# Optimization experiments

Hardware: AMD Instinct MI355X
Metric: run time of the kernel (lower is better)

## Reference

```python
import jax, jax.numpy as jnp
import numpy as np

N_NODES = 50000
HIDDEN = 256
N_EDGES = 800000


def setup_inputs() -> dict:
    key = jax.random.key(0)
    k_z, k_e, k_w1, k_b1, k_w2, k_b2 = jax.random.split(key, 6)
    z = jax.random.normal(k_z, (N_NODES, HIDDEN), dtype=jnp.float32)
    edge_index = jax.random.randint(k_e, (2, N_EDGES), 0, N_NODES, dtype=jnp.int64)
    # Linear params stored as (in, out); scaled like torch default init
    W1 = jax.random.normal(k_w1, (2 * HIDDEN, HIDDEN), dtype=jnp.float32) * (1.0 / np.sqrt(2 * HIDDEN))
    b1 = jax.random.normal(k_b1, (HIDDEN,), dtype=jnp.float32) * 0.01
    W2 = jax.random.normal(k_w2, (HIDDEN, 1), dtype=jnp.float32) * (1.0 / np.sqrt(HIDDEN))
    b2 = jax.random.normal(k_b2, (1,), dtype=jnp.float32) * 0.01
    return {"z": z, "edge_index": edge_index, "W1": W1, "b1": b1, "W2": W2, "b2": b2}


def reference(z, edge_index, W1, b1, W2, b2):
    src = edge_index[0]
    dst = edge_index[1]
    # gather endpoints and concat: [E, 2*H]
    edge_feat = jnp.concatenate([z[src], z[dst]], axis=1)
    x = jnp.dot(edge_feat, W1) + b1          # [E, H]
    x = jax.nn.relu(x)
    score = jnp.dot(x, W2) + b2              # [E, 1]
    return score
```

## Files before the change

### kernel.cpp

```cpp
#include <hip/hip_runtime.h>
#include <hip/hip_bf16.h>

#define NN 50000
#define HID 256
#define NE 800000

typedef unsigned short u16;
typedef __attribute__((ext_vector_type(8))) short short8v;
typedef __attribute__((ext_vector_type(4))) float f32x4;

__device__ __forceinline__ u16 f2bf(float v) {
    __hip_bfloat16 h = __float2bfloat16(v);
    return *reinterpret_cast<u16*>(&h);
}

__global__ __launch_bounds__(256)
void prep_w1b(const float* __restrict__ W1, u16* __restrict__ W1b) {
    const int g = blockIdx.x * 256 + threadIdx.x;
    if (g >= 2 * 32 * 256) return;
    const int h   = g >> 13;
    const int kbg = (g >> 8) & 31;
    const int jh  = g & 255;
    u16 o[8];
    #pragma unroll
    for (int kk = 0; kk < 8; ++kk)
        o[kk] = f2bf(W1[(size_t)(h * 256 + kbg * 8 + kk) * HID + jh]);
    *(uint4*)(W1b + (size_t)g * 8) = *(uint4*)o;
}

__global__ __launch_bounds__(512)
void node_gemm(const float* __restrict__ z, const u16* __restrict__ W1b,
               const float* __restrict__ b1, u16* __restrict__ P) {
    __shared__ __align__(16) u16 Blds[32 * 256 * 8];

    const int tid  = threadIdx.x;
    const int lane = tid & 63;
    const int w    = tid >> 6;
    const int l16  = lane & 15;
    const int l4   = lane >> 4;
    const int r0   = blockIdx.x * 256 + w * 32;

    short8v af[2][8];
    #pragma unroll
    for (int mi = 0; mi < 2; ++mi) {
        const int row = r0 + mi * 16 + l16;
        const bool ok = (row < NN);
        const float* zr = z + (size_t)row * HID;
        #pragma unroll
        for (int ks = 0; ks < 8; ++ks) {
            float4 v0 = make_float4(0.f, 0.f, 0.f, 0.f), v1 = v0;
            if (ok) {
                v0 = *(const float4*)(zr + ks * 32 + l4 * 8);
                v1 = *(const float4*)(zr + ks * 32 + l4 * 8 + 4);
            }
            u16 t[8] = { f2bf(v0.x), f2bf(v0.y), f2bf(v0.z), f2bf(v0.w),
                         f2bf(v1.x), f2bf(v1.y), f2bf(v1.z), f2bf(v1.w) };
            af[mi][ks] = *(short8v*)t;
        }
    }

    const uint4* Wu4 = (const uint4*)W1b;
    uint4* Lu4 = (uint4*)Blds;

    #pragma unroll
    for (int h = 0; h < 2; ++h) {
        if (h) __syncthreads();
        #pragma unroll
        for (int c = 0; c < 16; ++c)
            Lu4[c * 512 + tid] = Wu4[(size_t)h * 8192 + c * 512 + tid];
        __syncthreads();

        #pragma unroll
        for (int ni = 0; ni < 16; ++ni) {
            f32x4 acc[2] = {};
            #pragma unroll
            for (int ks = 0; ks < 8; ++ks) {
                const short8v b = *(const short8v*)
                    &Blds[((ks * 4 + l4) * 256 + ni * 16 + l16) * 8];
                #pragma unroll
                for (int mi = 0; mi < 2; ++mi)
                    acc[mi] = __builtin_amdgcn_mfma_f32_16x16x32_bf16(
                        af[mi][ks], b, acc[mi], 0, 0, 0);
            }
            const int col  = h * 256 + ni * 16 + l16;
            const float bias = (h == 0) ? b1[ni * 16 + l16] : 0.f;
            #pragma unroll
            for (int mi = 0; mi < 2; ++mi) {
                #pragma unroll
                for (int r = 0; r < 4; ++r) {
                    const int row = r0 + mi * 16 + l4 * 4 + r;
                    if (row < NN)
                        P[(size_t)row * 512 + col] = f2bf(acc[mi][r] + bias);
                }
            }
        }
    }
}

__device__ __forceinline__ void proc_pair(unsigned int ua, unsigned int ub,
                                          float w0, float w1, float& s) {
    const float a0 = __uint_as_float(ua << 16);
    const float a1 = __uint_as_float(ua & 0xffff0000u);
    const float b0 = __uint_as_float(ub << 16);
    const float b1 = __uint_as_float(ub & 0xffff0000u);
    const float x0 = fmaxf(a0 + b0, 0.f);
    const float x1 = fmaxf(a1 + b1, 0.f);
    s = fmaf(x0, w0, s);
    s = fmaf(x1, w1, s);
}

__global__ __launch_bounds__(256)
void edge_kernel(const int* __restrict__ ei, const u16* __restrict__ P,
                 const float* __restrict__ W2, const float* __restrict__ b2,
                 float* __restrict__ out) {
    const int lane = threadIdx.x & 63;
    const int sub  = lane >> 4;
    const int l16  = lane & 15;
    const int h0   = l16 * 16;

    float w[16];
    #pragma unroll
    for (int i = 0; i < 16; i += 4) {
        const float4 v = *(const float4*)(W2 + h0 + i);
        w[i] = v.x; w[i + 1] = v.y; w[i + 2] = v.z; w[i + 3] = v.w;
    }
    const float bias2 = b2[0];

    const int gwave   = (blockIdx.x * blockDim.x + threadIdx.x) >> 6;
    const int nwaves  = (gridDim.x * blockDim.x) >> 6;
    const int ngroups = NE >> 2;

    for (int g = gwave; g < ngroups; g += nwaves) {
        const int e   = g * 4 + sub;
        const int src = ei[e];
        const int dst = ei[NE + e];

        const u16* pa = P + (size_t)src * 512 + h0;
        const u16* pb = P + (size_t)dst * 512 + 256 + h0;
        const uint4 ta0 = *(const uint4*)(pa);
        const uint4 ta1 = *(const uint4*)(pa + 8);
        const uint4 tb0 = *(const uint4*)(pb);
        const uint4 tb1 = *(const uint4*)(pb + 8);

        float s = 0.f;
        proc_pair(ta0.x, tb0.x, w[0],  w[1],  s);
        proc_pair(ta0.y, tb0.y, w[2],  w[3],  s);
        proc_pair(ta0.z, tb0.z, w[4],  w[5],  s);
        proc_pair(ta0.w, tb0.w, w[6],  w[7],  s);
        proc_pair(ta1.x, tb1.x, w[8],  w[9],  s);
        proc_pair(ta1.y, tb1.y, w[10], w[11], s);
        proc_pair(ta1.z, tb1.z, w[12], w[13], s);
        proc_pair(ta1.w, tb1.w, w[14], w[15], s);

        s += __shfl_xor(s, 1);
        s += __shfl_xor(s, 2);
        s += __shfl_xor(s, 4);
        s += __shfl_xor(s, 8);
        if (l16 == 0) out[e] = s + bias2;
    }
}

extern "C" void kernel_launch(void* const* d_in, const int* in_sizes, int n_in,
                              void* d_out, int out_size, void* d_ws, size_t ws_size,
                              hipStream_t stream) {
    const float* z  = (const float*)d_in[0];
    const int*   ei = (const int*)d_in[1];
    const float* W1 = (const float*)d_in[2];
    const float* b1 = (const float*)d_in[3];
    const float* W2 = (const float*)d_in[4];
    const float* b2 = (const float*)d_in[5];
    float* out = (float*)d_out;

    u16* W1b = (u16*)d_ws;
    u16* P   = (u16*)d_ws + 131072;

    prep_w1b<<<64, 256, 0, stream>>>(W1, W1b);

    node_gemm<<<196, 512, 0, stream>>>(z, W1b, b1, P);

    edge_kernel<<<2048, 256, 0, stream>>>(ei, P, W2, b2, out);
}
```

Measured before the change: 240.7 us.

## Bucket-sort edges by dst/src tile and pin buckets to XCDs for cache locality

```diff
diff --git a/kernel.cpp b/kernel.cpp
--- a/kernel.cpp
+++ b/kernel.cpp
@@ -6,12 +6,23 @@
 #define NE 800000
 
 typedef unsigned short u16;
+typedef unsigned int u32;
+typedef unsigned long long u64;
 typedef __attribute__((ext_vector_type(8))) short short8v;
 typedef __attribute__((ext_vector_type(4))) float f32x4;
+typedef __attribute__((ext_vector_type(4))) u32 v4u;
+
+#define NBIN 512
 
 __device__ __forceinline__ u16 f2bf(float v) {
     __hip_bfloat16 h = __float2bfloat16(v);
     return *reinterpret_cast<u16*>(&h);
+}
+
+__device__ __forceinline__ u32 edge_key(int src, int dst) {
+    const u32 dt = (u32)(dst * 8) / 50000u;
+    const u32 st = (u32)(src * 64) / 50000u;
+    return dt * 64u + st;
 }
 
 __global__ __launch_bounds__(256)
@@ -97,7 +108,71 @@
     }
 }
 
-__device__ __forceinline__ void proc_pair(unsigned int ua, unsigned int ub,
+__global__ __launch_bounds__(256)
+void hist_kernel(const int* __restrict__ ei, u32* __restrict__ hist) {
+    __shared__ u32 h[NBIN];
+    for (int i = threadIdx.x; i < NBIN; i += 256) h[i] = 0;
+    __syncthreads();
+    for (int e = blockIdx.x * 256 + threadIdx.x; e < NE; e += gridDim.x * 256)
+        atomicAdd(&h[edge_key(ei[e], ei[NE + e])], 1u);
+    __syncthreads();
+    for (int i = threadIdx.x; i < NBIN; i += 256)
+        if (h[i]) atomicAdd(&hist[i], h[i]);
+}
+
+__global__ __launch_bounds__(512)
+void scan_kernel(u32* __restrict__ cursor, u32* __restrict__ offsets) {
+    __shared__ u32 s[NBIN];
+    const int tid = threadIdx.x;
+    const u32 mine = cursor[tid];
+    s[tid] = mine;
+    __syncthreads();
+    for (int off = 1; off < NBIN; off <<= 1) {
+        const u32 v = (tid >= off) ? s[tid - off] : 0u;
+        __syncthreads();
+        s[tid] += v;
+        __syncthreads();
+    }
+    const u32 excl = s[tid] - mine;
+    cursor[tid]  = excl;
+    offsets[tid] = excl;
+    if (tid == NBIN - 1) offsets[NBIN] = s[NBIN - 1];
+}
+
+__global__ __launch_bounds__(256)
+void scatter_kernel(const int* __restrict__ ei, u32* __restrict__ cursor,
+                    u64* __restrict__ packed) {
+    __shared__ u32 h[NBIN];
+    __shared__ u32 bb[NBIN];
+    for (int i = threadIdx.x; i < NBIN; i += 256) h[i] = 0;
+    __syncthreads();
+    const int e0 = blockIdx.x * 2048 + threadIdx.x;
+    u32 key[8], idx[8];
+    #pragma unroll
+    for (int i = 0; i < 8; ++i) {
+        const int e = e0 + i * 256;
+        key[i] = 0xFFFFFFFFu;
+        if (e < NE) {
+            key[i] = edge_key(ei[e], ei[NE + e]);
+            idx[i] = atomicAdd(&h[key[i]], 1u);
+        }
+    }
+    __syncthreads();
+    for (int i = threadIdx.x; i < NBIN; i += 256)
+        bb[i] = h[i] ? atomicAdd(&cursor[i], h[i]) : 0u;
+    __syncthreads();
+    #pragma unroll
+    for (int i = 0; i < 8; ++i) {
+        if (key[i] != 0xFFFFFFFFu) {
+            const int e = e0 + i * 256;
+            const u64 p = (u64)(u32)ei[e] | ((u64)(u32)ei[NE + e] << 17)
+                        | ((u64)(u32)e << 34);
+            packed[bb[key[i]] + idx[i]] = p;
+        }
+    }
+}
+
+__device__ __forceinline__ void proc_pair(u32 ua, u32 ub,
                                           float w0, float w1, float& s) {
     const float a0 = __uint_as_float(ua << 16);
     const float a1 = __uint_as_float(ua & 0xffff0000u);
@@ -110,9 +185,9 @@
 }
 
 __global__ __launch_bounds__(256)
-void edge_kernel(const int* __restrict__ ei, const u16* __restrict__ P,
-                 const float* __restrict__ W2, const float* __restrict__ b2,
-                 float* __restrict__ out) {
+void edge_sorted(const u64* __restrict__ packed, const u32* __restrict__ offsets,
+                 const u16* __restrict__ P, const float* __restrict__ W2,
+                 const float* __restrict__ b2, float* __restrict__ out) {
     const int lane = threadIdx.x & 63;
     const int sub  = lane >> 4;
     const int l16  = lane & 15;
@@ -126,19 +201,27 @@
     }
     const float bias2 = b2[0];
 
-    const int gwave   = (blockIdx.x * blockDim.x + threadIdx.x) >> 6;
-    const int nwaves  = (gridDim.x * blockDim.x) >> 6;
-    const int ngroups = NE >> 2;
-
-    for (int g = gwave; g < ngroups; g += nwaves) {
-        const int e   = g * 4 + sub;
-        const int src = ei[e];
-        const int dst = ei[NE + e];
-
-        const u16* pa = P + (size_t)src * 512 + h0;
+    const int xcd = blockIdx.x & 7;
+    const int sb  = blockIdx.x >> 3;
+    const u32 lo  = offsets[xcd * 64];
+    const u32 hi  = offsets[xcd * 64 + 64];
+    const int nb  = gridDim.x >> 3;
+    const int wib = sb * 4 + (threadIdx.x >> 6);
+    const u32 stride = (u32)nb * 4u * 4u;
+
+    for (u32 b4 = lo + (u32)wib * 4u; b4 < hi; b4 += stride) {
+        const u32 e4  = b4 + (u32)sub;
+        const bool act = (e4 < hi);
+        const u64 pk = act
+            ? __builtin_nontemporal_load(&packed[e4]) : 0ull;
+        const int src = (int)(pk & 0x1FFFFu);
+        const int dst = (int)((pk >> 17) & 0x1FFFFu);
+        const int eo  = (int)(pk >> 34);
+
+        const v4u* pa = (const v4u*)(P + (size_t)src * 512 + h0);
         const u16* pb = P + (size_t)dst * 512 + 256 + h0;
-        const uint4 ta0 = *(const uint4*)(pa);
-        const uint4 ta1 = *(const uint4*)(pa + 8);
+        const v4u ta0 = __builtin_nontemporal_load(pa);
+        const v4u ta1 = __builtin_nontemporal_load(pa + 1);
         const uint4 tb0 = *(const uint4*)(pb);
         const uint4 tb1 = *(const uint4*)(pb + 8);
 
@@ -156,9 +239,65 @@
         s += __shfl_xor(s, 2);
         s += __shfl_xor(s, 4);
         s += __shfl_xor(s, 8);
+        if (l16 == 0 && act) out[eo] = s + bias2;
+    }
+}
+
+__global__ __launch_bounds__(256)
+void edge_kernel(const int* __restrict__ ei, const u16* __restrict__ P,
+                 const float* __restrict__ W2, const float* __restrict__ b2,
+                 float* __restrict__ out) {
+    const int lane = threadIdx.x & 63;
+    const int sub  = lane >> 4;
+    const int l16  = lane & 15;
+    const int h0   = l16 * 16;
+
+    float w[16];
+    #pragma unroll
+    for (int i = 0; i < 16; i += 4) {
+        const float4 v = *(const float4*)(W2 + h0 + i);
+        w[i] = v.x; w[i + 1] = v.y; w[i + 2] = v.z; w[i + 3] = v.w;
+    }
+    const float bias2 = b2[0];
+
+    const int gwave   = (blockIdx.x * blockDim.x + threadIdx.x) >> 6;
+    const int nwaves  = (gridDim.x * blockDim.x) >> 6;
+    const int ngroups = NE >> 2;
+
+    for (int g = gwave; g < ngroups; g += nwaves) {
+        const int e   = g * 4 + sub;
+        const int src = ei[e];
+        const int dst = ei[NE + e];
+
+        const u16* pa = P + (size_t)src * 512 + h0;
+        const u16* pb = P + (size_t)dst * 512 + 256 + h0;
+        const uint4 ta0 = *(const uint4*)(pa);
+        const uint4 ta1 = *(const uint4*)(pa + 8);
+        const uint4 tb0 = *(const uint4*)(pb);
+        const uint4 tb1 = *(const uint4*)(pb + 8);
+
+        float s = 0.f;
+        proc_pair(ta0.x, tb0.x, w[0],  w[1],  s);
+        proc_pair(ta0.y, tb0.y, w[2],  w[3],  s);
+        proc_pair(ta0.z, tb0.z, w[4],  w[5],  s);
+        proc_pair(ta0.w, tb0.w, w[6],  w[7],  s);
+        proc_pair(ta1.x, tb1.x, w[8],  w[9],  s);
+        proc_pair(ta1.y, tb1.y, w[10], w[11], s);
+        proc_pair(ta1.z, tb1.z, w[12], w[13], s);
+        proc_pair(ta1.w, tb1.w, w[14], w[15], s);
+
+        s += __shfl_xor(s, 1);
+        s += __shfl_xor(s, 2);
+        s += __shfl_xor(s, 4);
+        s += __shfl_xor(s, 8);
         if (l16 == 0) out[e] = s + bias2;
     }
 }
+
+#define WS_PACKED   51462144u
+#define WS_CURSOR   57862144u
+#define WS_OFFSETS  57864192u
+#define WS_REQ      57866256u
 
 extern "C" void kernel_launch(void* const* d_in, const int* in_sizes, int n_in,
                               void* d_out, int out_size, void* d_ws, size_t ws_size,
@@ -171,12 +310,24 @@
     const float* b2 = (const float*)d_in[5];
     float* out = (float*)d_out;
 
-    u16* W1b = (u16*)d_ws;
-    u16* P   = (u16*)d_ws + 131072;
+    char* ws = (char*)d_ws;
+    u16* W1b = (u16*)ws;
+    u16* P   = (u16*)(ws + 262144);
 
     prep_w1b<<<64, 256, 0, stream>>>(W1, W1b);
-
     node_gemm<<<196, 512, 0, stream>>>(z, W1b, b1, P);
 
-    edge_kernel<<<2048, 256, 0, stream>>>(ei, P, W2, b2, out);
-}
+    if (ws_size >= WS_REQ) {
+        u64* packed  = (u64*)(ws + WS_PACKED);
+        u32* cursor  = (u32*)(ws + WS_CURSOR);
+        u32* offsets = (u32*)(ws + WS_OFFSETS);
+
+        hipMemsetAsync(cursor, 0, NBIN * sizeof(u32), stream);
+        hist_kernel<<<256, 256, 0, stream>>>(ei, cursor);
+        scan_kernel<<<1, NBIN, 0, stream>>>(cursor, offsets);
+        scatter_kernel<<<(NE + 2047) / 2048, 256, 0, stream>>>(ei, cursor, packed);
+        edge_sorted<<<1024, 256, 0, stream>>>(packed, offsets, P, W2, b2, out);
+    } else {
+        edge_kernel<<<2048, 256, 0, stream>>>(ei, P, W2, b2, out);
+    }
+}
```

Result: slower. 287.7 us (+19.5%).
